# Kernel tuning notes

Measured on AMD Instinct MI355X. Metric: run time of the kernel, lower is better.

## Reference

```python
import jax, jax.numpy as jnp
import numpy as np

N_NODES = 100000
IN_DIM = 512
HIDDEN = 64
NUM_CLASSES = 40
N_EDGES = 3200000


def setup_inputs() -> dict:
    key = jax.random.key(0)
    k1, k2, k3, k4, k5 = jax.random.split(key, 5)
    x = jax.random.normal(k1, (N_NODES, IN_DIM), dtype=jnp.float32)
    edge_index = jax.random.randint(k2, (2, N_EDGES), 0, N_NODES, dtype=jnp.int64)
    # Glorot init like PyG GCNConv, zero bias
    s1 = (6.0 / (IN_DIM + HIDDEN)) ** 0.5
    W1 = jax.random.uniform(k3, (IN_DIM, HIDDEN), jnp.float32, -s1, s1)
    b1 = jnp.zeros((HIDDEN,), jnp.float32)
    s2 = (6.0 / (HIDDEN + NUM_CLASSES)) ** 0.5
    W2 = jax.random.uniform(k4, (HIDDEN, NUM_CLASSES), jnp.float32, -s2, s2)
    b2 = jnp.zeros((NUM_CLASSES,), jnp.float32)
    return {"x": x, "edge_index": edge_index, "W1": W1, "b1": b1, "W2": W2, "b2": b2}


def _gcn_norm(edge_index, num_nodes):
    # Add self-loops, compute symmetric normalization D^-1/2 A D^-1/2 (PyG GCNConv default).
    loop = jnp.arange(num_nodes, dtype=edge_index.dtype)
    src = jnp.concatenate([edge_index[0], loop])
    dst = jnp.concatenate([edge_index[1], loop])
    deg = jax.ops.segment_sum(jnp.ones_like(src, dtype=jnp.float32), dst, num_segments=num_nodes)
    dinv = jnp.where(deg > 0, jax.lax.rsqrt(deg), 0.0)
    norm = dinv[src] * dinv[dst]  # [E+N]
    return src, dst, norm


def _gcn_conv(x, src, dst, norm, W, b, num_nodes):
    h = x @ W                                # [N, F_out]
    msg = h[src] * norm[:, None]             # gather + scale, [E+N, F_out]
    out = jax.ops.segment_sum(msg, dst, num_segments=num_nodes)  # scatter-add
    return out + b


def reference(x, edge_index, W1, b1, W2, b2):
    n = x.shape[0]
    src, dst, norm = _gcn_norm(edge_index, n)
    h = _gcn_conv(x, src, dst, norm, W1, b1, n)
    h = jax.nn.relu(h)
    # F.dropout(training=False) is identity in eval mode
    h = _gcn_conv(h, src, dst, norm, W2, b2, n)
    return jax.nn.log_softmax(h, axis=1)
```

## Files before the change

kernel.cpp:

```cpp
#include <hip/hip_runtime.h>
#include <hip/hip_bf16.h>
#include <cmath>

#define NN 100000
#define IND 512
#define HID 64
#define NC  40
#define BWN 256
#define NBKT ((NN + BWN - 1) / BWN)
#define NBIN_BLOCKS 100

typedef unsigned int uint32;
typedef unsigned short ushort;
using short8 = __attribute__((ext_vector_type(8))) short;
using f32x4  = __attribute__((ext_vector_type(4))) float;

__device__ inline float bf_lo(uint32 u) { return __uint_as_float(u << 16); }
__device__ inline float bf_hi(uint32 u) { return __uint_as_float(u & 0xFFFF0000u); }
__device__ inline uint32 f2bf(float f) {
    uint32 u = __float_as_uint(f);
    return (u + 0x7FFFu + ((u >> 16) & 1u)) >> 16;
}
__device__ inline uint32 pack2bf(float a, float b) { return f2bf(a) | (f2bf(b) << 16); }


__global__ __launch_bounds__(256) void zero_kernel(int* __restrict__ ghist, int n) {
    int i = blockIdx.x * blockDim.x + threadIdx.x;
    if (i < n) ghist[i] = 0;
}

__global__ __launch_bounds__(256) void bhist_kernel(const int* __restrict__ dst,
                                                    int* __restrict__ ghist, int E) {
    __shared__ int hist[NBKT];
    int t = threadIdx.x;
    for (int i = t; i < NBKT; i += 256) hist[i] = 0;
    __syncthreads();
    for (int e = blockIdx.x * 256 + t; e < E; e += gridDim.x * 256)
        atomicAdd(&hist[dst[e] >> 8], 1);
    __syncthreads();
    for (int i = t; i < NBKT; i += 256)
        if (hist[i]) atomicAdd(&ghist[i], hist[i]);
}

__global__ __launch_bounds__(512) void bscan_kernel(const int* __restrict__ ghist,
                                                    int* __restrict__ bbase,
                                                    int* __restrict__ gcursor) {
    __shared__ int sh[512];
    int t = threadIdx.x;
    int v = (t < NBKT) ? ghist[t] : 0;
    sh[t] = v;
    __syncthreads();
    for (int off = 1; off < 512; off <<= 1) {
        int u = (t >= off) ? sh[t - off] : 0;
        __syncthreads();
        sh[t] += u;
        __syncthreads();
    }
    int ex = sh[t] - v;
    if (t < NBKT) { bbase[t] = ex; gcursor[t] = ex; }
    if (t == NBKT - 1) bbase[NBKT] = ex + v;
}

__global__ __launch_bounds__(512) void bin_kernel(const int* __restrict__ src,
                                                  const int* __restrict__ dst,
                                                  int* __restrict__ gcursor,
                                                  int* __restrict__ packed, int E) {
    __shared__ int hist[NBKT], base[NBKT], cur[NBKT];
    int b = blockIdx.x, t = threadIdx.x;
    int epb = (E + gridDim.x - 1) / gridDim.x;
    int lo = b * epb;
    int hi = lo + epb; if (hi > E) hi = E;
    for (int i = t; i < NBKT; i += 512) { hist[i] = 0; cur[i] = 0; }
    __syncthreads();
    for (int e = lo + t; e < hi; e += 512) atomicAdd(&hist[dst[e] >> 8], 1);
    __syncthreads();
    for (int i = t; i < NBKT; i += 512)
        if (hist[i]) base[i] = atomicAdd(&gcursor[i], hist[i]);
    __syncthreads();
    for (int e = lo + t; e < hi; e += 512) {
        int d = dst[e], s = src[e];
        int bk = d >> 8;
        int pos = base[bk] + atomicAdd(&cur[bk], 1);
        packed[pos] = ((d & 255) << 17) | s;
    }
}

__global__ __launch_bounds__(256) void csr_bucket_kernel(const int* __restrict__ packed,
                                                         const int* __restrict__ bbase,
                                                         int* __restrict__ rowptr,
                                                         int* __restrict__ colx,
                                                         float* __restrict__ dinv, int E) {
    __shared__ int hist[BWN], pfx[BWN], cur[BWN];
    int b = blockIdx.x, t = threadIdx.x;
    int nlo = b * BWN;
    int ncnt = NN - nlo; if (ncnt > BWN) ncnt = BWN;
    int ebeg = bbase[b], eend = bbase[b + 1];
    hist[t] = 0;
    __syncthreads();
    for (int e = ebeg + t; e < eend; e += 256) atomicAdd(&hist[packed[e] >> 17], 1);
    __syncthreads();
    int h = hist[t];
    pfx[t] = h;
    __syncthreads();
    for (int off = 1; off < 256; off <<= 1) {
        int u = (t >= off) ? pfx[t - off] : 0;
        __syncthreads();
        pfx[t] += u;
        __syncthreads();
    }
    int excl = pfx[t] - h;
    cur[t] = excl;
    int g = nlo + t;
    if (t < ncnt) {
        rowptr[g] = ebeg + excl;
        dinv[g] = rsqrtf((float)(h + 1));
    }
    if (b == 0 && t == 0) rowptr[NN] = E;
    __syncthreads();
    for (int e = ebeg + t; e < eend; e += 256) {
        int p = packed[e];
        int dl = p >> 17;
        int s = p & 0x1FFFF;
        int pos = ebeg + atomicAdd(&cur[dl], 1);
        colx[pos] = s;
    }
}


__global__ __launch_bounds__(256) void w1t_kernel(const float* __restrict__ W1,
                                                  ushort* __restrict__ w1t) {
    int id = blockIdx.x * blockDim.x + threadIdx.x;
    if (id >= IND * HID) return;
    int n = id & 63, k = id >> 6;
    w1t[(size_t)n * IND + k] = (ushort)f2bf(W1[(size_t)k * HID + n]);
}


__global__ __launch_bounds__(256) void gemm1_mfma(const float* __restrict__ x,
                                                  const ushort* __restrict__ w1t,
                                                  const float* __restrict__ dinv,
                                                  ushort* __restrict__ hs, int M) {
    __shared__ ushort As[64 * 64];
    __shared__ ushort Bs[64 * 64];
    char* Ab = (char*)As;
    char* Bb = (char*)Bs;

    int t = threadIdx.x;
    int row0 = blockIdx.x * 64;

    int srow = t >> 2;
    int klane = t & 3;
    int grow = row0 + srow; if (grow > M - 1) grow = M - 1;
    const float* xrow = x + (size_t)grow * IND;
    const char* wrow = (const char*)(w1t + (size_t)srow * IND);
    int swrow = srow * 128;
    int swx = (srow & 7) << 4;

    int l = t & 63;
    int w = t >> 6;
    int lr = l & 15;
    int lk = (l >> 4) * 16;
    int arow_b = (w * 16 + lr) * 128;
    int aswz = ((w * 16 + lr) & 7) << 4;

    f32x4 acc[4] = {};

    for (int k0 = 0; k0 < IND; k0 += 64) {
#pragma unroll
        for (int i = 0; i < 4; ++i) {
            float4 v = *(const float4*)(xrow + k0 + i * 16 + klane * 4);
            uint2 pkd;
            pkd.x = pack2bf(v.x, v.y);
            pkd.y = pack2bf(v.z, v.w);
            int kb = i * 32 + klane * 8;
            *(uint2*)(Ab + swrow + (kb ^ swx)) = pkd;
            uint2 wv = *(const uint2*)(wrow + k0 * 2 + kb);
            *(uint2*)(Bb + swrow + (kb ^ swx)) = wv;
        }
        __syncthreads();

        short8 a0 = *(const short8*)(Ab + arow_b + ((0 + lk) ^ aswz));
        short8 a1 = *(const short8*)(Ab + arow_b + ((64 + lk) ^ aswz));
#pragma unroll
        for (int ns = 0; ns < 4; ++ns) {
            int brow = ns * 16 + lr;
            int bswz = (brow & 7) << 4;
            short8 b0 = *(const short8*)(Bb + brow * 128 + ((0 + lk) ^ bswz));
            short8 b1 = *(const short8*)(Bb + brow * 128 + ((64 + lk) ^ bswz));
            acc[ns] = __builtin_amdgcn_mfma_f32_16x16x32_bf16(a0, b0, acc[ns], 0, 0, 0);
            acc[ns] = __builtin_amdgcn_mfma_f32_16x16x32_bf16(a1, b1, acc[ns], 0, 0, 0);
        }
        __syncthreads();
    }

    int rbase = row0 + w * 16 + (l >> 4) * 4;
    float dv[4];
#pragma unroll
    for (int j = 0; j < 4; ++j) dv[j] = (rbase + j < M) ? dinv[rbase + j] : 0.f;
#pragma unroll
    for (int ns = 0; ns < 4; ++ns) {
        int col = ns * 16 + lr;
#pragma unroll
        for (int j = 0; j < 4; ++j) {
            int row = rbase + j;
            if (row < M) hs[(size_t)row * HID + col] = (ushort)f2bf(acc[ns][j] * dv[j]);
        }
    }
}


__global__ __launch_bounds__(256) void agg1_kernel(const uint32* __restrict__ hs,
                                                   const int* __restrict__ rowptr,
                                                   const int* __restrict__ colx,
                                                   const float* __restrict__ dinv,
                                                   const float* __restrict__ b1,
                                                   uint32* __restrict__ h1) {
    int node = (blockIdx.x * blockDim.x + threadIdx.x) >> 5;
    int l = threadIdx.x & 31;
    if (node >= NN) return;
    int beg = rowptr[node], end = rowptr[node + 1];
    uint32 u = hs[(size_t)node * 32 + l];
    float a0 = bf_lo(u), a1 = bf_hi(u);
    int e = beg;
    int n8 = beg + ((end - beg) & ~7);
    for (; e < n8; e += 8) {
        int c[8];
#pragma unroll
        for (int j = 0; j < 8; ++j) c[j] = colx[e + j];
        uint32 uu[8];
#pragma unroll
        for (int j = 0; j < 8; ++j) uu[j] = hs[(size_t)c[j] * 32 + l];
#pragma unroll
        for (int j = 0; j < 8; ++j) { a0 += bf_lo(uu[j]); a1 += bf_hi(uu[j]); }
    }
    for (; e < end; ++e) {
        uint32 ue = hs[(size_t)colx[e] * 32 + l];
        a0 += bf_lo(ue); a1 += bf_hi(ue);
    }
    float d = dinv[node];
    float2 bb = *(const float2*)(b1 + 2 * l);
    float v0 = a0 * d + bb.x;
    float v1 = a1 * d + bb.y;
    v0 = v0 > 0.f ? v0 : 0.f;
    v1 = v1 > 0.f ? v1 : 0.f;
    __builtin_nontemporal_store(pack2bf(v0, v1), &h1[(size_t)node * 32 + l]);
}


__global__ __launch_bounds__(256) void gemm2_kernel(const uint32* __restrict__ h1,
                                                    const float* __restrict__ W2,
                                                    const float* __restrict__ dinv,
                                                    ushort* __restrict__ h2b, int M) {
    __shared__ float hsld[64][68];
    __shared__ float wls[64 * 40];
    int tid = threadIdx.x;
    int row0 = blockIdx.x * 64;

    int r = tid >> 2;
    int q = tid & 3;
    int grow = row0 + r; if (grow > M - 1) grow = M - 1;
    const uint4* srcp = (const uint4*)(h1 + (size_t)grow * 32);
    uint4 q0 = srcp[q * 2];
    uint4 q1 = srcp[q * 2 + 1];
    uint32 wv[8] = {q0.x, q0.y, q0.z, q0.w, q1.x, q1.y, q1.z, q1.w};
#pragma unroll
    for (int jw = 0; jw < 8; ++jw) {
        hsld[r][q * 16 + 2 * jw]     = bf_lo(wv[jw]);
        hsld[r][q * 16 + 2 * jw + 1] = bf_hi(wv[jw]);
    }
    for (int idx = tid; idx < HID * NC; idx += 256) wls[idx] = W2[idx];
    __syncthreads();

    for (int o = tid; o < 64 * NC; o += 256) {
        int rr = o / NC;
        int c = o - rr * NC;
        float s = 0.f;
#pragma unroll
        for (int k4 = 0; k4 < 16; ++k4) {
            float4 hv = *(float4*)&hsld[rr][k4 * 4];
            s += hv.x * wls[(k4 * 4 + 0) * NC + c];
            s += hv.y * wls[(k4 * 4 + 1) * NC + c];
            s += hv.z * wls[(k4 * 4 + 2) * NC + c];
            s += hv.w * wls[(k4 * 4 + 3) * NC + c];
        }
        int row = row0 + rr;
        if (row < M) h2b[(size_t)row * NC + c] = (ushort)f2bf(s * dinv[row]);
    }
}


__global__ __launch_bounds__(256) void agg2_kernel(const uint32* __restrict__ h2b,
                                                   const int* __restrict__ rowptr,
                                                   const int* __restrict__ colx,
                                                   const float* __restrict__ dinv,
                                                   const float* __restrict__ b2,
                                                   float* __restrict__ out) {
    int node = (blockIdx.x * blockDim.x + threadIdx.x) >> 5;
    int l = threadIdx.x & 31;
    if (node >= NN) return;
    bool act = l < 20;
    int beg = rowptr[node], end = rowptr[node + 1];
    float a0 = 0.f, a1 = 0.f;
    if (act) {
        uint32 u = h2b[(size_t)node * 20 + l];
        a0 = bf_lo(u); a1 = bf_hi(u);
    }
    int e = beg;
    int n8 = beg + ((end - beg) & ~7);
    for (; e < n8; e += 8) {
        int c[8];
#pragma unroll
        for (int j = 0; j < 8; ++j) c[j] = colx[e + j];
        if (act) {
            uint32 uu[8];
#pragma unroll
            for (int j = 0; j < 8; ++j) uu[j] = h2b[(size_t)c[j] * 20 + l];
#pragma unroll
            for (int j = 0; j < 8; ++j) { a0 += bf_lo(uu[j]); a1 += bf_hi(uu[j]); }
        }
    }
    for (; e < end; ++e) {
        if (act) {
            uint32 ue = h2b[(size_t)colx[e] * 20 + l];
            a0 += bf_lo(ue); a1 += bf_hi(ue);
        }
    }

    float d = dinv[node];
    float v0 = -INFINITY, v1 = -INFINITY;
    if (act) {
        float2 bb = *(const float2*)(b2 + 2 * l);
        v0 = a0 * d + bb.x;
        v1 = a1 * d + bb.y;
    }
    float m = fmaxf(v0, v1);
#pragma unroll
    for (int off = 16; off; off >>= 1) m = fmaxf(m, __shfl_xor(m, off));
    float s = act ? (expf(v0 - m) + expf(v1 - m)) : 0.f;
#pragma unroll
    for (int off = 16; off; off >>= 1) s += __shfl_xor(s, off);
    if (act) {
        float ls = logf(s);
        __builtin_nontemporal_store(v0 - m - ls, &out[(size_t)node * NC + 2 * l]);
        __builtin_nontemporal_store(v1 - m - ls, &out[(size_t)node * NC + 2 * l + 1]);
    }
}


extern "C" void kernel_launch(void* const* d_in, const int* in_sizes, int n_in,
                              void* d_out, int out_size, void* d_ws, size_t ws_size,
                              hipStream_t stream) {
    const float* x  = (const float*)d_in[0];
    const int* ei   = (const int*)d_in[1];
    const float* W1 = (const float*)d_in[2];
    const float* b1 = (const float*)d_in[3];
    const float* W2 = (const float*)d_in[4];
    const float* b2 = (const float*)d_in[5];
    float* out = (float*)d_out;

    const int E = in_sizes[1] / 2;
    const int* src = ei;
    const int* dst = ei + E;

    char* p = (char*)d_ws;
    size_t off = 0;
    auto carve = [&](size_t bytes) {
        void* q = p + off;
        off = (off + bytes + 255) & ~(size_t)255;
        return q;
    };
    int* ghist    = (int*)carve((size_t)NBKT * 4);
    int* bbase    = (int*)carve((size_t)(NBKT + 1) * 4);
    int* gcursor  = (int*)carve((size_t)NBKT * 4);
    int* rowptr   = (int*)carve((size_t)(NN + 1) * 4);
    float* dinv   = (float*)carve((size_t)NN * 4);
    int* colx     = (int*)carve((size_t)E * 4);
    ushort* w1t   = (ushort*)carve((size_t)IND * HID * 2);
    ushort* hs    = (ushort*)carve((size_t)NN * HID * 2);
    ushort* h2b   = (ushort*)carve((size_t)NN * NC * 2);
    uint32* h1    = (uint32*)carve((size_t)NN * 32 * 4);
    int* packed   = (int*)carve((size_t)E * 4);

    zero_kernel<<<(NBKT + 255) / 256, 256, 0, stream>>>(ghist, NBKT);
    bhist_kernel<<<256, 256, 0, stream>>>(dst, ghist, E);
    bscan_kernel<<<1, 512, 0, stream>>>(ghist, bbase, gcursor);
    bin_kernel<<<NBIN_BLOCKS, 512, 0, stream>>>(src, dst, gcursor, packed, E);
    csr_bucket_kernel<<<NBKT, 256, 0, stream>>>(packed, bbase, rowptr, colx, dinv, E);
    w1t_kernel<<<(IND * HID + 255) / 256, 256, 0, stream>>>(W1, w1t);
    gemm1_mfma<<<(NN + 63) / 64, 256, 0, stream>>>(x, w1t, dinv, hs, NN);
    agg1_kernel<<<(NN * 32 + 255) / 256, 256, 0, stream>>>((const uint32*)hs, rowptr, colx, dinv, b1, h1);
    gemm2_kernel<<<(NN + 63) / 64, 256, 0, stream>>>(h1, W2, dinv, h2b, NN);
    agg2_kernel<<<(NN * 32 + 255) / 256, 256, 0, stream>>>((const uint32*)h2b, rowptr, colx, dinv, b2, out);
}
```

Measured before the change: 337.2 us.

## Use MFMA for second GEMM, prefetch GEMM1 tiles, nontemporal colx loads

Replaces the scalar FP32 LDS-based second GEMM with a bf16 MFMA kernel that reads h1 rows directly and uses a padded, transposed W2 built in a combined weight-transpose kernel. GEMM1 now register-prefetches the next K tile of x and W1 before computing the current one, so global loads overlap with MFMA work. Column-index loads in both aggregation kernels become nontemporal to reduce cache pollution. The cost is more registers in GEMM1 and bf16 inputs to the second GEMM.

New measurement: 339.3 us. About the same (+0.6%).

```diff
diff --git a/kernel.cpp b/kernel.cpp
--- a/kernel.cpp
+++ b/kernel.cpp
@@ -127,12 +127,19 @@
 }
 
 
-__global__ __launch_bounds__(256) void w1t_kernel(const float* __restrict__ W1,
-                                                  ushort* __restrict__ w1t) {
+__global__ __launch_bounds__(256) void wt_kernel(const float* __restrict__ W1,
+                                                 const float* __restrict__ W2,
+                                                 ushort* __restrict__ w1t,
+                                                 ushort* __restrict__ w2t) {
     int id = blockIdx.x * blockDim.x + threadIdx.x;
-    if (id >= IND * HID) return;
-    int n = id & 63, k = id >> 6;
-    w1t[(size_t)n * IND + k] = (ushort)f2bf(W1[(size_t)k * HID + n]);
+    if (id < IND * HID) {
+        int n = id & 63, k = id >> 6;
+        w1t[(size_t)n * IND + k] = (ushort)f2bf(W1[(size_t)k * HID + n]);
+    } else if (id < IND * HID + 48 * HID) {
+        int id2 = id - IND * HID;
+        int n = id2 >> 6, k = id2 & 63;
+        w2t[id2] = (n < NC) ? (ushort)f2bf(W2[(size_t)k * NC + n]) : (ushort)0;
+    }
 }
 
 
@@ -165,19 +172,32 @@
 
     f32x4 acc[4] = {};
 
+    float4 rx[4]; uint2 rw[4];
+#pragma unroll
+    for (int i = 0; i < 4; ++i) {
+        rx[i] = *(const float4*)(xrow + i * 16 + klane * 4);
+        rw[i] = *(const uint2*)(wrow + i * 32 + klane * 8);
+    }
+
     for (int k0 = 0; k0 < IND; k0 += 64) {
 #pragma unroll
         for (int i = 0; i < 4; ++i) {
-            float4 v = *(const float4*)(xrow + k0 + i * 16 + klane * 4);
+            int kb = i * 32 + klane * 8;
             uint2 pkd;
-            pkd.x = pack2bf(v.x, v.y);
-            pkd.y = pack2bf(v.z, v.w);
-            int kb = i * 32 + klane * 8;
+            pkd.x = pack2bf(rx[i].x, rx[i].y);
+            pkd.y = pack2bf(rx[i].z, rx[i].w);
             *(uint2*)(Ab + swrow + (kb ^ swx)) = pkd;
-            uint2 wv = *(const uint2*)(wrow + k0 * 2 + kb);
-            *(uint2*)(Bb + swrow + (kb ^ swx)) = wv;
-        }
-        __syncthreads();
+            *(uint2*)(Bb + swrow + (kb ^ swx)) = rw[i];
+        }
+        __syncthreads();
+
+        if (k0 + 64 < IND) {
+#pragma unroll
+            for (int i = 0; i < 4; ++i) {
+                rx[i] = *(const float4*)(xrow + k0 + 64 + i * 16 + klane * 4);
+                rw[i] = *(const uint2*)(wrow + (k0 + 64) * 2 + i * 32 + klane * 8);
+            }
+        }
 
         short8 a0 = *(const short8*)(Ab + arow_b + ((0 + lk) ^ aswz));
         short8 a1 = *(const short8*)(Ab + arow_b + ((64 + lk) ^ aswz));
@@ -226,7 +246,7 @@
     for (; e < n8; e += 8) {
         int c[8];
 #pragma unroll
-        for (int j = 0; j < 8; ++j) c[j] = colx[e + j];
+        for (int j = 0; j < 8; ++j) c[j] = __builtin_nontemporal_load(&colx[e + j]);
         uint32 uu[8];
 #pragma unroll
         for (int j = 0; j < 8; ++j) uu[j] = hs[(size_t)c[j] * 32 + l];
@@ -234,7 +254,7 @@
         for (int j = 0; j < 8; ++j) { a0 += bf_lo(uu[j]); a1 += bf_hi(uu[j]); }
     }
     for (; e < end; ++e) {
-        uint32 ue = hs[(size_t)colx[e] * 32 + l];
+        uint32 ue = hs[(size_t)__builtin_nontemporal_load(&colx[e]) * 32 + l];
         a0 += bf_lo(ue); a1 += bf_hi(ue);
     }
     float d = dinv[node];
@@ -247,44 +267,42 @@
 }
 
 
-__global__ __launch_bounds__(256) void gemm2_kernel(const uint32* __restrict__ h1,
-                                                    const float* __restrict__ W2,
-                                                    const float* __restrict__ dinv,
-                                                    ushort* __restrict__ h2b, int M) {
-    __shared__ float hsld[64][68];
-    __shared__ float wls[64 * 40];
-    int tid = threadIdx.x;
-    int row0 = blockIdx.x * 64;
-
-    int r = tid >> 2;
-    int q = tid & 3;
-    int grow = row0 + r; if (grow > M - 1) grow = M - 1;
-    const uint4* srcp = (const uint4*)(h1 + (size_t)grow * 32);
-    uint4 q0 = srcp[q * 2];
-    uint4 q1 = srcp[q * 2 + 1];
-    uint32 wv[8] = {q0.x, q0.y, q0.z, q0.w, q1.x, q1.y, q1.z, q1.w};
-#pragma unroll
-    for (int jw = 0; jw < 8; ++jw) {
-        hsld[r][q * 16 + 2 * jw]     = bf_lo(wv[jw]);
-        hsld[r][q * 16 + 2 * jw + 1] = bf_hi(wv[jw]);
-    }
-    for (int idx = tid; idx < HID * NC; idx += 256) wls[idx] = W2[idx];
-    __syncthreads();
-
-    for (int o = tid; o < 64 * NC; o += 256) {
-        int rr = o / NC;
-        int c = o - rr * NC;
-        float s = 0.f;
-#pragma unroll
-        for (int k4 = 0; k4 < 16; ++k4) {
-            float4 hv = *(float4*)&hsld[rr][k4 * 4];
-            s += hv.x * wls[(k4 * 4 + 0) * NC + c];
-            s += hv.y * wls[(k4 * 4 + 1) * NC + c];
-            s += hv.z * wls[(k4 * 4 + 2) * NC + c];
-            s += hv.w * wls[(k4 * 4 + 3) * NC + c];
-        }
-        int row = row0 + rr;
-        if (row < M) h2b[(size_t)row * NC + c] = (ushort)f2bf(s * dinv[row]);
+__global__ __launch_bounds__(256) void gemm2_mfma(const ushort* __restrict__ h1,
+                                                  const ushort* __restrict__ w2t,
+                                                  const float* __restrict__ dinv,
+                                                  ushort* __restrict__ h2b, int M) {
+    int t = threadIdx.x;
+    int w = t >> 6, l = t & 63;
+    int lr = l & 15, lh = l >> 4;
+    int row0 = blockIdx.x * 64 + w * 16;
+    int arow = row0 + lr; if (arow > M - 1) arow = M - 1;
+    const ushort* hrow = h1 + (size_t)arow * HID;
+
+    f32x4 acc[3] = {};
+#pragma unroll
+    for (int ks = 0; ks < 2; ++ks) {
+        short8 a = *(const short8*)(hrow + ks * 32 + lh * 8);
+#pragma unroll
+        for (int ns = 0; ns < 3; ++ns) {
+            short8 b = *(const short8*)(w2t + (size_t)(ns * 16 + lr) * HID + ks * 32 + lh * 8);
+            acc[ns] = __builtin_amdgcn_mfma_f32_16x16x32_bf16(a, b, acc[ns], 0, 0, 0);
+        }
+    }
+
+    int rbase = row0 + lh * 4;
+    float dv[4];
+#pragma unroll
+    for (int j = 0; j < 4; ++j) dv[j] = (rbase + j < M) ? dinv[rbase + j] : 0.f;
+#pragma unroll
+    for (int ns = 0; ns < 3; ++ns) {
+        int col = ns * 16 + lr;
+        if (col < NC) {
+#pragma unroll
+            for (int j = 0; j < 4; ++j) {
+                int row = rbase + j;
+                if (row < M) h2b[(size_t)row * NC + col] = (ushort)f2bf(acc[ns][j] * dv[j]);
+            }
+        }
     }
 }
 
@@ -310,7 +328,7 @@
     for (; e < n8; e += 8) {
         int c[8];
 #pragma unroll
-        for (int j = 0; j < 8; ++j) c[j] = colx[e + j];
+        for (int j = 0; j < 8; ++j) c[j] = __builtin_nontemporal_load(&colx[e + j]);
         if (act) {
             uint32 uu[8];
 #pragma unroll
@@ -320,8 +338,9 @@
         }
     }
     for (; e < end; ++e) {
+        int c = __builtin_nontemporal_load(&colx[e]);
         if (act) {
-            uint32 ue = h2b[(size_t)colx[e] * 20 + l];
+            uint32 ue = h2b[(size_t)c * 20 + l];
             a0 += bf_lo(ue); a1 += bf_hi(ue);
         }
     }
@@ -376,6 +395,7 @@
     float* dinv   = (float*)carve((size_t)NN * 4);
     int* colx     = (int*)carve((size_t)E * 4);
     ushort* w1t   = (ushort*)carve((size_t)IND * HID * 2);
+    ushort* w2t   = (ushort*)carve((size_t)48 * HID * 2);
     ushort* hs    = (ushort*)carve((size_t)NN * HID * 2);
     ushort* h2b   = (ushort*)carve((size_t)NN * NC * 2);
     uint32* h1    = (uint32*)carve((size_t)NN * 32 * 4);
@@ -386,9 +406,9 @@
     bscan_kernel<<<1, 512, 0, stream>>>(ghist, bbase, gcursor);
     bin_kernel<<<NBIN_BLOCKS, 512, 0, stream>>>(src, dst, gcursor, packed, E);
     csr_bucket_kernel<<<NBKT, 256, 0, stream>>>(packed, bbase, rowptr, colx, dinv, E);
-    w1t_kernel<<<(IND * HID + 255) / 256, 256, 0, stream>>>(W1, w1t);
+    wt_kernel<<<(IND * HID + 48 * HID + 255) / 256, 256, 0, stream>>>(W1, W2, w1t, w2t);
     gemm1_mfma<<<(NN + 63) / 64, 256, 0, stream>>>(x, w1t, dinv, hs, NN);
     agg1_kernel<<<(NN * 32 + 255) / 256, 256, 0, stream>>>((const uint32*)hs, rowptr, colx, dinv, b1, h1);
-    gemm2_kernel<<<(NN + 63) / 64, 256, 0, stream>>>(h1, W2, dinv, h2b, NN);
+    gemm2_mfma<<<(NN + 63) / 64, 256, 0, stream>>>((const ushort*)h1, w2t, dinv, h2b, NN);
     agg2_kernel<<<(NN * 32 + 255) / 256, 256, 0, stream>>>((const uint32*)h2b, rowptr, colx, dinv, b2, out);
 }
```
